# Kernel optimization log

Hardware: AMD Instinct MI355X
Metric: run time of the kernel (lower is better)

The kernel has to match this reference:

```python
import jax, jax.numpy as jnp
import numpy as np

B, HH, WW, C = 8, 56, 56, 192
DEPTH = 2
D_IN = 384      # ssm_ratio=2.0 * d_model
R = 12          # dt_rank = ceil(192/16)
HID = 768
L = HH * WW
EPS = 1e-5

PNAMES = ("norm1_w", "norm1_b", "in_proj_w", "conv_w", "conv_b", "x_proj_w",
          "dt_proj_w", "dt_proj_b", "A_log", "Ds", "out_norm_w", "out_norm_b",
          "out_proj_w", "norm2_w", "norm2_b", "fc1_w", "fc1_b", "fc2_w", "fc2_b")


def _mst_bfs_np(fm):
    """Per-image MST (Kruskal) on the 4-connected grid with cosine-distance
    edge weights mapped through exp (MinimumSpanningTree('Cosine', torch.exp)),
    then BFS from node 0. Returns (bfs order, parent-of-ordered-node)."""
    fm = np.asarray(fm, np.float32)
    Bn, H, W, Cc = fm.shape
    Ln = H * W
    idx_out = np.zeros((Bn, Ln), np.int32)
    par_out = np.zeros((Bn, Ln), np.int32)
    ids = np.arange(Ln).reshape(H, W)
    e_u = np.concatenate([ids[:, :-1].ravel(), ids[:-1, :].ravel()])
    e_v = np.concatenate([ids[:, 1:].ravel(), ids[1:, :].ravel()])
    for b in range(Bn):
        f = fm[b].reshape(Ln, Cc)
        nrm = np.linalg.norm(f, axis=1) + 1e-8
        cos = (f[e_u] * f[e_v]).sum(1) / (nrm[e_u] * nrm[e_v])
        wgt = np.exp(1.0 - cos)
        order = np.argsort(wgt, kind="stable")
        uf = np.arange(Ln)
        def find(a):
            while uf[a] != a:
                uf[a] = uf[uf[a]]
                a = uf[a]
            return a
        adj = [[] for _ in range(Ln)]
        cnt = 0
        for e in order:
            u, v = int(e_u[e]), int(e_v[e])
            ru, rv = find(u), find(v)
            if ru != rv:
                uf[ru] = rv
                adj[u].append(v)
                adj[v].append(u)
                cnt += 1
                if cnt == Ln - 1:
                    break
        bfs = np.zeros(Ln, np.int32)
        par = np.zeros(Ln, np.int32)
        visited = np.zeros(Ln, bool)
        visited[0] = True
        head, tail = 0, 1
        while head < tail:
            u = int(bfs[head])
            for v in adj[u]:
                if not visited[v]:
                    visited[v] = True
                    bfs[tail] = v
                    par[tail] = u
                    tail += 1
            head += 1
        idx_out[b] = bfs
        par_out[b] = par
    return idx_out, par_out


def _mst_bfs(x):
    shp = jax.ShapeDtypeStruct((x.shape[0], x.shape[1] * x.shape[2]), jnp.int32)
    return jax.pure_callback(_mst_bfs_np, (shp, shp), jax.lax.stop_gradient(x))


def _ln(x, w, b):
    mu = jnp.mean(x, -1, keepdims=True)
    var = jnp.mean((x - mu) ** 2, -1, keepdims=True)
    return (x - mu) * jax.lax.rsqrt(var + EPS) * w + b


def _tree_scan(feat, w, bfs_idx, bfs_par):
    # feat, w: (B, L, D); bfs_idx/bfs_par: (B, L) int32.
    # Pass 1 (leaf->root): S[p] += w[n] * S[n] in reverse BFS order.
    # Pass 2 (root->leaf): H[n] = S[n] + w[n] * (H[p] - w[n] * S[n]).
    Bn = feat.shape[0]
    bi = jnp.arange(Bn)

    def p1(S, np_):
        n, p = np_
        S = S.at[bi, p].add(w[bi, n] * S[bi, n])
        return S, None

    xs1 = (bfs_idx[:, 1:][:, ::-1].T, bfs_par[:, 1:][:, ::-1].T)
    S, _ = jax.lax.scan(p1, feat, xs1)

    def p2(Hc, np_):
        n, p = np_
        wn, sn = w[bi, n], S[bi, n]
        Hc = Hc.at[bi, n].set(sn + wn * (Hc[bi, p] - wn * sn))
        return Hc, None

    xs2 = (bfs_idx[:, 1:].T, bfs_par[:, 1:].T)
    Hh, _ = jax.lax.scan(p2, S, xs2)
    return Hh


def _layer(x, p, tree):
    bfs_idx, bfs_par = tree
    Bn = x.shape[0]
    # --- Tree_SSM branch (pre-norm) ---
    xn = _ln(x, p["norm1_w"], p["norm1_b"])
    xz = xn @ p["in_proj_w"].T                     # (B,H,W,2*D_IN)
    xs, z = jnp.split(xz, 2, axis=-1)
    xs = jax.lax.conv_general_dilated(
        xs, p["conv_w"], (1, 1), "SAME",
        dimension_numbers=("NHWC", "HWIO", "NHWC"),
        feature_group_count=D_IN) + p["conv_b"]    # depthwise 3x3
    u = jax.nn.silu(xs).reshape(Bn, L, D_IN)       # (B,L,D)
    x_dbl = u @ p["x_proj_w"].T                    # (B,L,R+2), d_state=1
    dts = jax.nn.softplus(x_dbl[..., :R] @ p["dt_proj_w"].T + p["dt_proj_b"])
    Bs, Cs = x_dbl[..., R:R + 1], x_dbl[..., R + 1:R + 2]
    A = -jnp.exp(p["A_log"][:, 0])                 # (D,)
    w = jnp.exp(dts * A)                           # edge decay to parent
    feat = dts * Bs * u                            # delta * B * u
    Hh = _tree_scan(feat, w, bfs_idx, bfs_par)
    y = (Cs * Hh + p["Ds"] * u).reshape(Bn, HH, WW, D_IN)
    y = _ln(y, p["out_norm_w"], p["out_norm_b"]) * jax.nn.silu(z)
    x = x + y @ p["out_proj_w"].T
    # --- MLP branch ---
    h = _ln(x, p["norm2_w"], p["norm2_b"])
    h = jax.nn.gelu(h @ p["fc1_w"].T + p["fc1_b"], approximate=False)
    return x + h @ p["fc2_w"].T + p["fc2_b"]


def setup_inputs() -> dict:
    key = jax.random.key(0)
    ks = jax.random.split(key, 12)
    n = jax.random.normal
    return {
        "x": n(ks[0], (B, HH, WW, C), jnp.float32),
        "norm1_w": jnp.ones((DEPTH, C)), "norm1_b": jnp.zeros((DEPTH, C)),
        "in_proj_w": n(ks[1], (DEPTH, 2 * D_IN, C)) * 0.02,
        "conv_w": n(ks[2], (DEPTH, 3, 3, 1, D_IN)) * 0.05,
        "conv_b": jnp.zeros((DEPTH, D_IN)),
        "x_proj_w": n(ks[3], (DEPTH, R + 2, D_IN)) * 0.02,
        "dt_proj_w": n(ks[4], (DEPTH, D_IN, R)) * 0.05,
        "dt_proj_b": n(ks[5], (DEPTH, D_IN)) * 0.1,
        "A_log": jnp.log(0.5 + jax.random.uniform(ks[6], (DEPTH, D_IN, 1))),
        "Ds": jax.random.uniform(ks[7], (DEPTH, D_IN)),
        "out_norm_w": jnp.ones((DEPTH, D_IN)), "out_norm_b": jnp.zeros((DEPTH, D_IN)),
        "out_proj_w": n(ks[8], (DEPTH, C, D_IN)) * 0.02,
        "norm2_w": jnp.ones((DEPTH, C)), "norm2_b": jnp.zeros((DEPTH, C)),
        "fc1_w": n(ks[9], (DEPTH, HID, C)) * 0.02, "fc1_b": jnp.zeros((DEPTH, HID)),
        "fc2_w": n(ks[10], (DEPTH, C, HID)) * 0.02, "fc2_b": jnp.zeros((DEPTH, C)),
        "fnorm_w": jnp.ones((C,)), "fnorm_b": jnp.zeros((C,)),
    }


def reference(x, norm1_w, norm1_b, in_proj_w, conv_w, conv_b, x_proj_w,
              dt_proj_w, dt_proj_b, A_log, Ds, out_norm_w, out_norm_b,
              out_proj_w, norm2_w, norm2_b, fc1_w, fc1_b, fc2_w, fc2_b,
              fnorm_w, fnorm_b):
    pvals = (norm1_w, norm1_b, in_proj_w, conv_w, conv_b, x_proj_w, dt_proj_w,
             dt_proj_b, A_log, Ds, out_norm_w, out_norm_b, out_proj_w, norm2_w,
             norm2_b, fc1_w, fc1_b, fc2_w, fc2_b)
    for i in range(DEPTH):
        pl = {k: v[i] for k, v in zip(PNAMES, pvals)}
        tree = _mst_bfs(x)  # input-adaptive MST, recomputed per layer
        x = _layer(x, pl, tree)
    return _ln(x, fnorm_w, fnorm_b)
```

## Files before the change

kernel.cpp:

```cpp
#include <hip/hip_runtime.h>
#include <math.h>

#define NB 8
#define NC 192
#define DIN 384
#define NL 3136
#define ROWS (NB*NL)
#define NE 6160
#define NHID 768

typedef unsigned short u16;
typedef unsigned int u32;
typedef unsigned long long u64;
typedef __attribute__((ext_vector_type(8))) short bh8;
typedef __attribute__((ext_vector_type(4))) float f4;

typedef __attribute__((address_space(1))) const void gl_as1;
typedef __attribute__((address_space(3))) void gl_as3;
#define GL16(g, l) __builtin_amdgcn_global_load_lds((gl_as1*)(const void*)(g), (gl_as3*)(void*)(l), 16, 0, 0)

__device__ __forceinline__ float wredsum(float v){
  v += __shfl_xor(v, 1, 64); v += __shfl_xor(v, 2, 64); v += __shfl_xor(v, 4, 64);
  v += __shfl_xor(v, 8, 64); v += __shfl_xor(v, 16, 64); v += __shfl_xor(v, 32, 64);
  return v;
}
__device__ __forceinline__ void edge_decode(int e, int& u, int& v){
  if (e < 3080){ int h = e/55, w = e - h*55; u = h*56 + w; v = u + 1; }
  else { int e2 = e - 3080; int h = e2/56, w = e2 - h*56; u = h*56 + w; v = u + 56; }
}
__device__ __forceinline__ float siluf(float x){ return x / (1.0f + expf(-x)); }
__device__ __forceinline__ float sofplus(float x){ return fmaxf(x, 0.0f) + log1pf(expf(-fabsf(x))); }
__device__ __forceinline__ float geluf(float x){ return 0.5f * x * (1.0f + erff(x * 0.70710678118654752f)); }
__device__ __forceinline__ u16 f2bf(float x){
  u32 u = __float_as_uint(x);
  u32 r = (u + 0x7fffu + ((u >> 16) & 1u)) >> 16;
  return (u16)r;
}
__device__ __forceinline__ float bf2f(u16 h){ return __uint_as_float(((u32)h) << 16); }

__global__ __launch_bounds__(256) void keysln_kernel(const float* __restrict__ x,
    const float* __restrict__ g, const float* __restrict__ bt,
    u16* __restrict__ lnout, u64* __restrict__ keys,
    const float* __restrict__ ipw, const float* __restrict__ opw,
    const float* __restrict__ f1w, const float* __restrict__ f2w,
    u16* __restrict__ ipo, u16* __restrict__ opo, u16* __restrict__ f1o, u16* __restrict__ f2o){
  int bid = blockIdx.x;
  int lane = threadIdx.x & 63;
  if (bid < 6272){
    int gw = (int)((bid * 256u + threadIdx.x) >> 6);
    const float* r = x + (size_t)gw * NC;
    float v[3]; float s = 0.f;
#pragma unroll
    for (int j = 0; j < 3; ++j){ v[j] = r[lane + 64*j]; s += v[j]; }
    s = wredsum(s);
    float mu = s * (1.0f / NC);
    float q = 0.f;
#pragma unroll
    for (int j = 0; j < 3; ++j){ float dd = v[j] - mu; q += dd*dd; }
    q = wredsum(q);
    float rs = rsqrtf(q * (1.0f / NC) + 1e-5f);
    u16* o = lnout + (size_t)gw * NC;
#pragma unroll
    for (int j = 0; j < 3; ++j){
      int dch = lane + 64*j;
      o[dch] = f2bf((v[j] - mu) * rs * g[dch] + bt[dch]);
    }
  } else if (bid < 18592){
    int gw = (int)(((bid - 6272) * 256u + threadIdx.x) >> 6);
    if (gw >= NB * NE) return;
    int b = gw / NE, e = gw - b * NE;
    int u, v; edge_decode(e, u, v);
    const float* ru = x + ((size_t)b * NL + u) * NC;
    const float* rv = x + ((size_t)b * NL + v) * NC;
    float s = 0.f, su = 0.f, sv = 0.f;
#pragma unroll
    for (int j = 0; j < 3; ++j){
      float a = ru[lane + 64*j], c = rv[lane + 64*j];
      s += a * c; su += a * a; sv += c * c;
    }
    s = wredsum(s);
    su = wredsum(su);
    sv = wredsum(sv);
    if (lane == 0){
      float nu = sqrtf(su) + 1e-8f;
      float nv = sqrtf(sv) + 1e-8f;
      float cosv = s / (nu * nv);
      float wgt = expf(1.0f - cosv);
      keys[(size_t)b*NE + e] = ((u64)__float_as_uint(wgt) << 32) | (u64)(u32)e;
    }
  } else {
    int wb = bid - 18592;
    const float* W; u16* o; int K; int nk; int base;
    if (wb < 576){ W = ipw; o = ipo; K = 192; nk = 768*192; base = wb; }
    else if (wb < 864){ W = opw; o = opo; K = 384; nk = 192*384; base = wb - 576; }
    else if (wb < 1440){ W = f1w; o = f1o; K = 192; nk = 768*192; base = wb - 864; }
    else { W = f2w; o = f2o; K = 768; nk = 192*768; base = wb - 1440; }
    int i = base*256 + threadIdx.x;
    if (i >= nk) return;
    int r = i / K, c = i - r*K;
    float v = W[i];
    u16 hi = f2bf(v);
    o[(size_t)r * 2 * K + c] = hi;
    o[(size_t)r * 2 * K + K + c] = f2bf(v - bf2f(hi));
  }
}

__device__ void tree_body(char* sm, int b, const u64* __restrict__ keys_g,
      int* __restrict__ order_g, int* __restrict__ parpos_g, int* __restrict__ pos_g,
      int* __restrict__ lvl_g, int* __restrict__ nlev_g){
  const int t = threadIdx.x;
  const int NT = 256;
  u64* best   = (u64*)sm;
  u16* parent = (u16*)(sm + 25088);
  u16* comp   = (u16*)(sm + 31360);
  u16* mstU   = (u16*)(sm + 37632);
  u16* mstV   = (u16*)(sm + 43904);
  u32* cnts   = (u32*)(sm + 56448);
  u16* adjl4  = (u16*)sm;
  u32* deg    = (u32*)(sm + 25088);
  u32* fr     = (u32*)(sm + 37632);
  u16* ppos   = (u16*)(sm + 50176);

  const u64* kb = keys_g + (size_t)b * NE;
  for (int v = t; v < NL; v += NT) parent[v] = (u16)v;
  if (t == 0){ cnts[0] = 0; cnts[3] = 0xffffffffu; }
  __syncthreads();

  u32 gpass = 0;
  for (int round = 0; round < 24; ++round){
    for (int it = 0; it < 12; ++it){
      bool ch = false;
      for (int c0 = 0; c0 < NL; c0 += NT*4){
        int vv[4]; u16 pv[4]; int nb2 = 0;
#pragma unroll
        for (int j = 0; j < 4; ++j){ int v = c0 + t + j*NT; if (v < NL){ vv[nb2] = v; pv[nb2] = parent[v]; ++nb2; } }
        u16 gp[4];
        for (int j = 0; j < nb2; ++j) gp[j] = parent[pv[j]];
        for (int j = 0; j < nb2; ++j){ if (gp[j] != pv[j]){ parent[vv[j]] = gp[j]; ch = true; } }
      }
      bool docheck = (it & 1);
      if (docheck && ch) cnts[3] = gpass;
      __syncthreads();
      if (docheck){
        u32 seen = cnts[3];
        __syncthreads();
        u32 cur = gpass; ++gpass;
        if (seen != cur) break;
      }
    }
    for (int v = t; v < NL; v += NT){ comp[v] = parent[v]; best[v] = ~0ull; }
    if (t == 0) cnts[2] = 0;
    __syncthreads();
    for (int c0 = 0; c0 < NE; c0 += NT*8){
      int ee[8]; int eu[8], ev[8]; u16 cu[8], cv[8]; u64 kk[8]; int nb2 = 0;
#pragma unroll
      for (int j = 0; j < 8; ++j){
        int e = c0 + t + j*NT;
        if (e < NE){ ee[nb2] = e; int u, v; edge_decode(e, u, v); eu[nb2] = u; ev[nb2] = v; ++nb2; }
      }
      for (int j = 0; j < nb2; ++j){ cu[j] = comp[eu[j]]; cv[j] = comp[ev[j]]; }
      for (int j = 0; j < nb2; ++j){ kk[j] = kb[ee[j]]; }
      for (int j = 0; j < nb2; ++j){
        if (cu[j] != cv[j]){
          atomicMin(&best[cu[j]], kk[j]);
          atomicMin(&best[cv[j]], kk[j]);
        }
      }
    }
    __syncthreads();
    for (int c0 = 0; c0 < NL; c0 += NT*4){
      int rr[4]; u64 bk[4]; int nb2 = 0;
#pragma unroll
      for (int j = 0; j < 4; ++j){ int r = c0 + t + j*NT; if (r < NL){ rr[nb2] = r; ++nb2; } }
      u16 cr[4];
      for (int j = 0; j < nb2; ++j) cr[j] = comp[rr[j]];
      for (int j = 0; j < nb2; ++j) bk[j] = (cr[j] == (u16)rr[j]) ? best[rr[j]] : ~0ull;
      int uu[4], vv2[4]; u16 ru2[4], rv2[4];
      for (int j = 0; j < nb2; ++j){
        if (bk[j] != ~0ull){ int e = (int)(u32)bk[j]; edge_decode(e, uu[j], vv2[j]); }
      }
      for (int j = 0; j < nb2; ++j){
        if (bk[j] != ~0ull){ ru2[j] = comp[uu[j]]; rv2[j] = comp[vv2[j]]; }
      }
      for (int j = 0; j < nb2; ++j){
        if (bk[j] != ~0ull){
          int r = rr[j];
          u16 other = (ru2[j] == (u16)r) ? rv2[j] : ru2[j];
          bool mutual = (best[other] == bk[j]);
          if (!mutual || (u16)r < other){
            parent[r] = other;
            u32 id = atomicAdd(&cnts[0], 1);
            mstU[id] = (u16)uu[j]; mstV[id] = (u16)vv2[j];
            cnts[2] = 1;
          }
        }
      }
    }
    __syncthreads();
    if (cnts[0] >= (u32)(NL - 1) || cnts[2] == 0) break;
  }
  __syncthreads();

  const int nm = NL - 1;
  for (int v = t; v < NL; v += NT){
    deg[v] = 0;
    *(u64*)&adjl4[v*4] = 0xffffffffffffffffull;
  }
  __syncthreads();
  for (int c0 = 0; c0 < nm; c0 += NT*4){
    int uu[4], vv2[4]; int nb2 = 0;
#pragma unroll
    for (int j = 0; j < 4; ++j){
      int i = c0 + t + j*NT;
      if (i < nm){ uu[nb2] = mstU[i]; vv2[nb2] = mstV[i]; ++nb2; }
    }
    for (int j = 0; j < nb2; ++j){
      u32 s1 = atomicAdd(&deg[uu[j]], 1); adjl4[uu[j]*4 + s1] = (u16)vv2[j];
      u32 s2 = atomicAdd(&deg[vv2[j]], 1); adjl4[vv2[j]*4 + s2] = (u16)uu[j];
    }
  }
  __syncthreads();

  if (t == 0){
    fr[0] = 0u | (0xffffu << 16);
    ppos[0] = 0;
    cnts[1] = 1;
    lvl_g[b*3200 + 0] = 0; lvl_g[b*3200 + 1] = 1;
  }
  __syncthreads();
  if (t < 64){
    int flo = 0, fhi = 1, d = 1;
    while (fhi < NL){
      for (int base2 = flo; base2 < fhi; base2 += 64){
        int idx = base2 + t;
        if (idx < fhi){
          u32 f = fr[idx];
          int u = (int)(f & 0xffffu), pn = (int)(f >> 16);
          u64 four = *(const u64*)&adjl4[u*4];
#pragma unroll
          for (int j = 0; j < 4; ++j){
            int v = (int)((four >> (16*j)) & 0xffffu);
            if (v != 0xffff && v != pn){
              u32 pos = atomicAdd(&cnts[1], 1);
              fr[pos] = (u32)v | ((u32)u << 16);
              ppos[pos] = (u16)idx;
            }
          }
        }
        asm volatile("s_waitcnt lgkmcnt(0)" ::: "memory");
      }
      int nf = (int)cnts[1];
      if (t == 0) lvl_g[b*3200 + d + 1] = nf;
      flo = fhi; fhi = nf; ++d;
      if (nf == flo) break;
    }
    if (t == 0) nlev_g[b] = d;
  }
  __syncthreads();

  for (int p = t; p < NL; p += NT){
    u32 f = fr[p];
    int node = (int)(f & 0xffffu);
    order_g[b*NL + p] = node;
    parpos_g[b*NL + p] = (int)ppos[p];
    pos_g[b*NL + node] = p;
  }
}

__device__ void inproj_body(char* sm, int bid, const u16* __restrict__ Ap, const u16* __restrict__ Wp,
                            float* __restrict__ Cm, float* __restrict__ C2){
  const int K = 192, K2 = 384;
  short* Ah = (short*)sm;
  short* Wh = (short*)(sm + 16384);
  short* Wl = (short*)(sm + 32768);
  const int bn = (bid % 6) * 128, bm = (bid / 6) * 128;
  const int tid = threadIdx.x, lane = tid & 63, wid = tid >> 6;
  const int wr = wid >> 1, wc = wid & 1;
  f4 acc[4][4];
#pragma unroll
  for (int mf = 0; mf < 4; ++mf)
#pragma unroll
    for (int nf = 0; nf < 4; ++nf) acc[mf][nf] = (f4){0.f,0.f,0.f,0.f};

  for (int k0 = 0; k0 < K; k0 += 64){
#pragma unroll
    for (int j = 0; j < 4; ++j){
      int isb = wid*4 + j;
      int r = isb*8 + (lane >> 3);
      int c = lane & 7;
      const u16* src = Ap + (size_t)(bm + r) * K + k0 + ((c ^ (r & 7)) << 3);
      GL16(src, &Ah[isb*512]);
    }
#pragma unroll
    for (int j = 0; j < 4; ++j){
      int isb = wid*4 + j;
      int r = isb*8 + (lane >> 3);
      int c = lane & 7;
      const u16* src = Wp + (size_t)(bn + r) * K2 + k0 + ((c ^ (r & 7)) << 3);
      GL16(src,     &Wh[isb*512]);
      GL16(src + K, &Wl[isb*512]);
    }
    __syncthreads();
#pragma unroll
    for (int kk = 0; kk < 2; ++kk){
      bh8 whf[4], wlf[4], ahf[4];
#pragma unroll
      for (int nf = 0; nf < 4; ++nf){
        int rw = wc*64 + nf*16 + (lane & 15);
        int c = kk*4 + (lane >> 4);
        int ad = rw*64 + ((c ^ (rw & 7)) * 8);
        whf[nf] = *(const bh8*)&Wh[ad];
        wlf[nf] = *(const bh8*)&Wl[ad];
      }
#pragma unroll
      for (int mf = 0; mf < 4; ++mf){
        int ra = wr*64 + mf*16 + (lane & 15);
        int c = kk*4 + (lane >> 4);
        int ad = ra*64 + ((c ^ (ra & 7)) * 8);
        ahf[mf] = *(const bh8*)&Ah[ad];
      }
#pragma unroll
      for (int mf = 0; mf < 4; ++mf)
#pragma unroll
        for (int nf = 0; nf < 4; ++nf){
          acc[mf][nf] = __builtin_amdgcn_mfma_f32_16x16x32_bf16(ahf[mf], whf[nf], acc[mf][nf], 0, 0, 0);
          acc[mf][nf] = __builtin_amdgcn_mfma_f32_16x16x32_bf16(ahf[mf], wlf[nf], acc[mf][nf], 0, 0, 0);
        }
    }
    __syncthreads();
  }
  const int cb = bn + wc*64;
#pragma unroll
  for (int mf = 0; mf < 4; ++mf){
    int row = bm + wr*64 + mf*16 + (lane >> 4)*4;
#pragma unroll
    for (int nf = 0; nf < 4; ++nf){
      int col = cb + nf*16 + (lane & 15);
#pragma unroll
      for (int r = 0; r < 4; ++r){
        float v = acc[mf][nf][r];
        float* op = (col < 384) ? Cm : C2;
        int oc = (col < 384) ? col : col - 384;
        op[(size_t)(row + r) * 384 + oc] = v;
      }
    }
  }
}

__global__ __launch_bounds__(256) void fused_tree_inproj(
    const u64* __restrict__ keysg, int* __restrict__ ordg, int* __restrict__ ppg,
    int* __restrict__ posg, int* __restrict__ lvlg, int* __restrict__ nlvg,
    const u16* __restrict__ Ap, const u16* __restrict__ Wp,
    float* __restrict__ Cm, float* __restrict__ C2){
  __shared__ __align__(16) char sm[62736];
  int bid = blockIdx.x;
  if (bid < 8){
    tree_body(sm, bid, keysg, ordg, ppg, posg, lvlg, nlvg);
  } else {
    inproj_body(sm, bid - 8, Ap, Wp, Cm, C2);
  }
}

__global__ __launch_bounds__(256) void sched_conv_kernel(
    const int* __restrict__ lvl_g, const int* __restrict__ nlev_g,
    u32* __restrict__ wsched_g, int* __restrict__ nwin_g,
    const float* __restrict__ xs, const float* __restrict__ cw,
    const float* __restrict__ cb, float* __restrict__ u){
  __shared__ int lvls[3200];
  int bid = blockIdx.x;
  if (bid < 8){
    int b = bid;
    int tid = threadIdx.x;
    int d = nlev_g[b];
    for (int i = tid; i <= d; i += 256) lvls[i] = lvl_g[b*3200 + i];
    __syncthreads();
    if (tid >= 64) return;
    int lane = tid;
    u32* su = wsched_g + (size_t)b*6528;
    u32* sd = su + 3264;
    int nk = d - 1;
    for (int pass = 0; pass < 2; ++pass){
      u32* out = pass ? sd : su;
      int carry = 0;
      for (int c0 = 0; c0 < nk; c0 += 64){
        int kk = c0 + lane;
        bool valid = kk < nk;
        int lo = 0, hi = 0, wc = 0;
        if (valid){
          int dd = pass ? (1 + kk) : (d - 1 - kk);
          lo = lvls[dd]; hi = lvls[dd+1];
          wc = (hi - lo + 63) >> 6;
        }
        int inc = wc;
        for (int off = 1; off < 64; off <<= 1){
          int v = __shfl_up(inc, off, 64);
          if (lane >= off) inc += v;
        }
        int excl = carry + inc - wc;
        if (valid){
          for (int w = 0; w < wc; ++w){
            int base2 = lo + (w << 6);
            u32 e = (u32)base2 | ((u32)hi << 16);
            if (base2 + 64 >= hi) e |= 0x80000000u;
            out[excl + w] = e;
          }
        }
        carry += __shfl(inc, 63, 64);
      }
      if (lane == 0) nwin_g[b*2 + pass] = carry;
    }
  } else {
    int idx = (bid - 8) * 256 + threadIdx.x;
    if (idx >= ROWS * 96) return;
    int q = idx % 96; int l = idx / 96;
    int b = l / NL; int hw = l - b * NL; int h = hw / 56; int wcc = hw - h * 56;
    int c4 = q * 4;
    float4 acc = *(const float4*)(cb + c4);
#pragma unroll
    for (int kh = 0; kh < 3; ++kh){
      int hh = h + kh - 1; if (hh < 0 || hh >= 56) continue;
#pragma unroll
      for (int kw = 0; kw < 3; ++kw){
        int wwc = wcc + kw - 1; if (wwc < 0 || wwc >= 56) continue;
        float4 iv = *(const float4*)(xs + ((size_t)(b * NL + hh*56 + wwc)) * DIN + c4);
        float4 wv = *(const float4*)(cw + (size_t)(kh*3 + kw) * DIN + c4);
        acc.x += iv.x * wv.x; acc.y += iv.y * wv.y; acc.z += iv.z * wv.z; acc.w += iv.w * wv.w;
      }
    }
    float4 o; o.x = siluf(acc.x); o.y = siluf(acc.y); o.z = siluf(acc.z); o.w = siluf(acc.w);
    *(float4*)(u + (size_t)l * DIN + c4) = o;
  }
}

template<int D, bool BF16OUT>
__global__ __launch_bounds__(256) void ln_kernel(const float* __restrict__ in, const float* __restrict__ g,
                                                 const float* __restrict__ bt, void* __restrict__ outv){
  int gw = (int)((blockIdx.x * 256u + threadIdx.x) >> 6);
  int lane = threadIdx.x & 63;
  if (gw >= ROWS) return;
  constexpr int J = D / 64;
  const float* r = in + (size_t)gw * D;
  float v[J]; float s = 0.f;
#pragma unroll
  for (int j = 0; j < J; ++j){ v[j] = r[lane + 64*j]; s += v[j]; }
  s = wredsum(s);
  float mu = s * (1.0f / D);
  float q = 0.f;
#pragma unroll
  for (int j = 0; j < J; ++j){ float dd = v[j] - mu; q += dd*dd; }
  q = wredsum(q);
  float rs = rsqrtf(q * (1.0f / D) + 1e-5f);
  if (BF16OUT){
    u16* o = (u16*)outv + (size_t)gw * D;
#pragma unroll
    for (int j = 0; j < J; ++j){
      int dch = lane + 64*j;
      float y = (v[j] - mu) * rs * g[dch] + bt[dch];
      o[dch] = f2bf(y);
    }
  } else {
    float* o = (float*)outv + (size_t)gw * D;
#pragma unroll
    for (int j = 0; j < J; ++j){ int dch = lane + 64*j; o[dch] = (v[j] - mu) * rs * g[dch] + bt[dch]; }
  }
}

template<int BN, bool BIAS, int ACT, bool RESID, bool OBF16, bool DUALOUT>
__global__ __launch_bounds__(256) void mgemm_kernel(
    const u16* __restrict__ Ap, const u16* __restrict__ Wp,
    const float* __restrict__ bias, const float* __restrict__ resid,
    float* __restrict__ Cm, float* __restrict__ C2, int M, int N, int K){
  static_assert(BN == 64 || BN == 128, "BN");
  constexpr int WT = (BN == 128) ? 64 : 32;
  constexpr int NF = WT / 16;
  __shared__ short Ah[128*64];
  __shared__ short Wh[BN*64], Wl[BN*64];
  const int bm = blockIdx.y * 128, bn = blockIdx.x * BN;
  const int tid = threadIdx.x, lane = tid & 63, wid = tid >> 6;
  const int wr = wid >> 1, wc = wid & 1;
  const int K2 = 2 * K;
  f4 acc[4][NF];
#pragma unroll
  for (int mf = 0; mf < 4; ++mf)
#pragma unroll
    for (int nf = 0; nf < NF; ++nf) acc[mf][nf] = (f4){0.f,0.f,0.f,0.f};

  for (int k0 = 0; k0 < K; k0 += 64){
#pragma unroll
    for (int j = 0; j < 4; ++j){
      int isb = wid*4 + j;
      int r = isb*8 + (lane >> 3);
      int c = lane & 7;
      const u16* src = Ap + (size_t)(bm + r) * K + k0 + ((c ^ (r & 7)) << 3);
      GL16(src, &Ah[isb*512]);
    }
#pragma unroll
    for (int j = 0; j < BN/32; ++j){
      int isb = wid*(BN/32) + j;
      int r = isb*8 + (lane >> 3);
      int c = lane & 7;
      const u16* src = Wp + (size_t)(bn + r) * K2 + k0 + ((c ^ (r & 7)) << 3);
      GL16(src,     &Wh[isb*512]);
      GL16(src + K, &Wl[isb*512]);
    }
    __syncthreads();
#pragma unroll
    for (int kk = 0; kk < 2; ++kk){
      bh8 whf[NF], wlf[NF], ahf[4];
#pragma unroll
      for (int nf = 0; nf < NF; ++nf){
        int rw = wc*WT + nf*16 + (lane & 15);
        int c = kk*4 + (lane >> 4);
        int ad = rw*64 + ((c ^ (rw & 7)) * 8);
        whf[nf] = *(const bh8*)&Wh[ad];
        wlf[nf] = *(const bh8*)&Wl[ad];
      }
#pragma unroll
      for (int mf = 0; mf < 4; ++mf){
        int ra = wr*64 + mf*16 + (lane & 15);
        int c = kk*4 + (lane >> 4);
        int ad = ra*64 + ((c ^ (ra & 7)) * 8);
        ahf[mf] = *(const bh8*)&Ah[ad];
      }
#pragma unroll
      for (int mf = 0; mf < 4; ++mf)
#pragma unroll
        for (int nf = 0; nf < NF; ++nf){
          acc[mf][nf] = __builtin_amdgcn_mfma_f32_16x16x32_bf16(ahf[mf], whf[nf], acc[mf][nf], 0, 0, 0);
          acc[mf][nf] = __builtin_amdgcn_mfma_f32_16x16x32_bf16(ahf[mf], wlf[nf], acc[mf][nf], 0, 0, 0);
        }
    }
    __syncthreads();
  }
  const int cb = bn + wc*WT;
#pragma unroll
  for (int mf = 0; mf < 4; ++mf){
    int row = bm + wr*64 + mf*16 + (lane >> 4)*4;
#pragma unroll
    for (int nf = 0; nf < NF; ++nf){
      int col = cb + nf*16 + (lane & 15);
#pragma unroll
      for (int r = 0; r < 4; ++r){
        float v = acc[mf][nf][r];
        if (BIAS) v += bias[col];
        if (ACT == 1) v = geluf(v);
        if (RESID) v += resid[(size_t)(row + r) * N + col];
        if (DUALOUT){
          float* op = (col < 384) ? Cm : C2;
          int oc = (col < 384) ? col : col - 384;
          op[(size_t)(row + r) * 384 + oc] = v;
        } else if (OBF16){
          u16* op = (u16*)Cm;
          op[(size_t)(row + r) * N + col] = f2bf(v);
        } else {
          Cm[(size_t)(row + r) * N + col] = v;
        }
      }
    }
  }
}

__global__ __launch_bounds__(256) void xdbl_kernel(const float* __restrict__ u,
    const float* __restrict__ xpw, const float* __restrict__ dtw_g,
    const float* __restrict__ dtb, const float* __restrict__ alog, const int* __restrict__ pos_g,
    float* __restrict__ wout, float* __restrict__ fout, float* __restrict__ csout){
  __shared__ float xw[14*384];
  __shared__ float dw[384*12];
  __shared__ float db[384];
  __shared__ float An[384];
  int t = threadIdx.x;
  for (int i = t; i < 14*384; i += 256) xw[i] = xpw[i];
  for (int i = t; i < 384*12; i += 256) dw[i] = dtw_g[i];
  for (int i = t; i < 384; i += 256){ db[i] = dtb[i]; An[i] = -expf(alog[i]); }
  __syncthreads();
  int wave = t >> 6, lane = t & 63;
  int row0 = blockIdx.x * 16 + wave * 4;
  for (int rr = 0; rr < 4; ++rr){
    int m = row0 + rr;
    int b = m / NL;
    int pos = pos_g[m];
    size_t orow = ((size_t)b * NL + pos) * DIN;
    const float* ur = u + (size_t)m * DIN;
    float u6[6];
#pragma unroll
    for (int j = 0; j < 6; ++j) u6[j] = ur[lane + 64*j];
    float xd[14];
#pragma unroll
    for (int r = 0; r < 14; ++r){
      float p = 0.f;
#pragma unroll
      for (int j = 0; j < 6; ++j) p += u6[j] * xw[r*384 + lane + 64*j];
      xd[r] = wredsum(p);
    }
    float Bs = xd[12], Cv = xd[13];
#pragma unroll
    for (int j = 0; j < 6; ++j){
      int dch = lane + 64*j;
      float pre = db[dch];
#pragma unroll
      for (int r = 0; r < 12; ++r) pre += xd[r] * dw[dch*12 + r];
      float dts = sofplus(pre);
      float wv = expf(dts * An[dch]);
      float fv = dts * Bs * u6[j];
      wout[orow + dch] = wv;
      fout[orow + dch] = fv;
    }
    if (lane == 0) csout[m] = Cv;
  }
}

__global__ __launch_bounds__(256) void wtr_kernel(const float* __restrict__ in, float* __restrict__ out){
  __shared__ float tile[64][65];
  int blk = blockIdx.x;
  int b = blk / (49*6);
  int r = blk - b*(49*6);
  int pt = r / 6, ct = r - pt*6;
  int t = threadIdx.x;
  int tr = t >> 6, lane = t & 63;
  const float* src = in + ((size_t)b*NL + (size_t)pt*64) * DIN + ct*64;
#pragma unroll
  for (int k = 0; k < 16; ++k){
    int rr = tr + k*4;
    tile[rr][lane] = src[(size_t)rr*DIN + lane];
  }
  __syncthreads();
  float* dst = out + ((size_t)b*DIN + (size_t)ct*64) * NL + (size_t)pt*64;
#pragma unroll
  for (int k = 0; k < 16; ++k){
    int cc = tr + k*4;
    dst[(size_t)cc*NL + lane] = tile[lane][cc];
  }
}

template<bool UP>
__device__ __forceinline__ void sweep_run(const u32* __restrict__ sc, int nw,
    float* __restrict__ Sp, const float* __restrict__ wbase, const int* __restrict__ pg, int lane){
  if (nw <= 0) return;
  u32 d0 = sc[lane];
  u32 d1 = sc[64 + lane];
  int curch = 0;
  float wA = 0.f, wB = 0.f; int pA = 0, pB = 0;
  int baseA = 0, hiA = 0, baseB = 0, hiB = 0;
  u32 eA = 0, eB = 0; bool aA = false, aB = false;
  {
    u32 dc = __shfl(d0, 0, 64);
    baseA = (int)(dc & 0xffffu); hiA = (int)((dc >> 16) & 0x7fffu); eA = dc >> 31;
    int p = baseA + lane; aA = p < hiA;
    if (aA){ wA = wbase[p]; pA = pg[p]; }
  }
  if (nw > 1){
    u32 dc = __shfl(d0, 1, 64);
    baseB = (int)(dc & 0xffffu); hiB = (int)((dc >> 16) & 0x7fffu); eB = dc >> 31;
    int p = baseB + lane; aB = p < hiB;
    if (aB){ wB = wbase[p]; pB = pg[p]; }
  }
  for (int iw = 0; iw < nw; ++iw){
    int ch = iw >> 6;
    if (ch != curch){ d0 = d1; d1 = sc[(ch + 1)*64 + lane]; curch = ch; }
    float wN = 0.f; int pN = 0; int baseN = 0, hiN = 0; u32 eN = 0; bool aN = false;
    int iw2 = iw + 2;
    if (iw2 < nw){
      int ch2 = iw2 >> 6;
      u32 dc2 = __shfl((ch2 == curch) ? d0 : d1, iw2 & 63, 64);
      baseN = (int)(dc2 & 0xffffu); hiN = (int)((dc2 >> 16) & 0x7fffu); eN = dc2 >> 31;
      int p = baseN + lane; aN = p < hiN;
      if (aN){ wN = wbase[p]; pN = pg[p]; }
    }
    int p = baseA + lane;
    if (aA){
      if (UP){
        float s = Sp[p];
        atomicAdd(&Sp[pA], wA * s);
      } else {
        float s = Sp[p]; float h = Sp[pA];
        Sp[p] = s + wA * (h - wA * s);
      }
    }
    if (eA){
      asm volatile("s_waitcnt lgkmcnt(0)" ::: "memory");
    }
    baseA = baseB; hiA = hiB; aA = aB; wA = wB; pA = pB; eA = eB;
    baseB = baseN; hiB = hiN; aB = aN; wB = wN; pB = pN; eB = eN;
  }
}

__global__ __launch_bounds__(256) void sweep8_kernel(const float* __restrict__ featp, const float* __restrict__ wtr,
    float* __restrict__ Hp, const int* __restrict__ parpos_g,
    const u32* __restrict__ wsched_g, const int* __restrict__ nwin_g){
  __shared__ float S[4*NL];
  int blk = blockIdx.x;
  int b = blk & 7, q = blk >> 3;
  int t = threadIdx.x, lane = t & 63, wv = t >> 6;
  const int* pg = parpos_g + b*NL;
  const float* fbase = featp + (size_t)b*NL*DIN + q*4;
  const float* wbase = wtr + ((size_t)b*DIN + q*4 + wv) * NL;
  float*       hbase = Hp    + (size_t)b*NL*DIN + q*4;
  for (int i = t; i < NL; i += 256){
    float4 f = *(const float4*)(fbase + (size_t)i*DIN);
    S[0*NL + i] = f.x; S[1*NL + i] = f.y; S[2*NL + i] = f.z; S[3*NL + i] = f.w;
  }
  __syncthreads();
  float* Sp = &S[wv*NL];

  const u32* su = wsched_g + (size_t)b*6528;
  const u32* sd = su + 3264;
  int nwu = nwin_g[b*2], nwd = nwin_g[b*2 + 1];
  sweep_run<true>(su, nwu, Sp, wbase, pg, lane);
  sweep_run<false>(sd, nwd, Sp, wbase, pg, lane);

  __syncthreads();
  for (int i = t; i < NL; i += 256){
    float4 o;
    o.x = S[0*NL + i]; o.y = S[1*NL + i]; o.z = S[2*NL + i]; o.w = S[3*NL + i];
    *(float4*)(hbase + (size_t)i*DIN) = o;
  }
}

__global__ __launch_bounds__(256) void ynorm_kernel(const float* __restrict__ Hp, const float* __restrict__ u,
    const float* __restrict__ z, const float* __restrict__ Cs, const int* __restrict__ order_g,
    const float* __restrict__ Ds, const float* __restrict__ g, const float* __restrict__ bt,
    u16* __restrict__ out){
  int gw = (int)((blockIdx.x * 256u + threadIdx.x) >> 6);
  int lane = threadIdx.x & 63;
  if (gw >= ROWS) return;
  int b = gw / NL;
  int node = order_g[gw];
  size_t nrow = (size_t)b * NL + node;
  float Cv = Cs[nrow];
  const float* hr = Hp + (size_t)gw * DIN;
  const float* ur = u + nrow * DIN;
  const float* zr = z + nrow * DIN;
  float y[6]; float s = 0.f;
#pragma unroll
  for (int j = 0; j < 6; ++j){
    int dch = lane + 64*j;
    y[j] = Cv * hr[dch] + Ds[dch] * ur[dch];
    s += y[j];
  }
  s = wredsum(s);
  float mu = s * (1.0f / DIN);
  float q = 0.f;
#pragma unroll
  for (int j = 0; j < 6; ++j){ float dd = y[j] - mu; q += dd*dd; }
  q = wredsum(q);
  float rs = rsqrtf(q * (1.0f / DIN) + 1e-5f);
  u16* o = out + nrow * DIN;
#pragma unroll
  for (int j = 0; j < 6; ++j){
    int dch = lane + 64*j;
    float yn = (y[j] - mu) * rs * g[dch] + bt[dch];
    float v = yn * siluf(zr[dch]);
    o[dch] = f2bf(v);
  }
}

extern "C" void kernel_launch(void* const* d_in, const int* in_sizes, int n_in,
                              void* d_out, int out_size, void* d_ws, size_t ws_size,
                              hipStream_t stream){
  const float* x_in       = (const float*)d_in[0];
  const float* norm1_w    = (const float*)d_in[1];
  const float* norm1_b    = (const float*)d_in[2];
  const float* in_proj_w  = (const float*)d_in[3];
  const float* conv_w     = (const float*)d_in[4];
  const float* conv_b     = (const float*)d_in[5];
  const float* x_proj_w   = (const float*)d_in[6];
  const float* dt_proj_w  = (const float*)d_in[7];
  const float* dt_proj_b  = (const float*)d_in[8];
  const float* A_log      = (const float*)d_in[9];
  const float* Ds         = (const float*)d_in[10];
  const float* out_norm_w = (const float*)d_in[11];
  const float* out_norm_b = (const float*)d_in[12];
  const float* out_proj_w = (const float*)d_in[13];
  const float* norm2_w    = (const float*)d_in[14];
  const float* norm2_b    = (const float*)d_in[15];
  const float* fc1_w      = (const float*)d_in[16];
  const float* fc1_b      = (const float*)d_in[17];
  const float* fc2_w      = (const float*)d_in[18];
  const float* fc2_b      = (const float*)d_in[19];
  const float* fnorm_w    = (const float*)d_in[20];
  const float* fnorm_b    = (const float*)d_in[21];

  float* ws = (float*)d_ws;
  float* X     = ws + 0;
  u16*   bufAh = (u16*)(ws + 4816896);
  float* bufZ  = ws + 9633792;
  float* bufW  = ws + 19267584;
  float* bufU  = ws + 28901376;
  float* bufF  = ws + 38535168;
  u16*   Gp    = (u16*)bufU;
  float* Csb   = ws + 48168960;
  int*   ordg  = (int*)(ws + 48194048);
  int*   ppg   = (int*)(ws + 48219136);
  int*   lvlg  = (int*)(ws + 48244224);
  int*   nlvg  = (int*)(ws + 48269824);
  u64*   keysg = (u64*)(ws + 48269832);
  u16*   ipWp  = (u16*)(ws + 48393480);
  u16*   opWp  = (u16*)(ws + 48540936);
  u16*   fc1Wp = (u16*)(ws + 48614664);
  u16*   fc2Wp = (u16*)(ws + 48762120);
  int*   posg  = (int*)(ws + 48909576);
  float* wtrp  = ws + 48934664;
  u32*   wschg = (u32*)(ws + 58568456);
  int*   nwing = (int*)(ws + 58620680);

  hipMemcpyAsync(X, x_in, (size_t)ROWS * NC * sizeof(float), hipMemcpyDeviceToDevice, stream);

  for (int i = 0; i < 2; ++i){
    keysln_kernel<<<20608, 256, 0, stream>>>(X, norm1_w + i*NC, norm1_b + i*NC, bufAh, keysg,
                                             in_proj_w + (size_t)i*NHID*NC, out_proj_w + (size_t)i*NC*DIN,
                                             fc1_w + (size_t)i*NHID*NC, fc2_w + (size_t)i*NC*NHID,
                                             ipWp, opWp, fc1Wp, fc2Wp);

    fused_tree_inproj<<<8 + 6*196, 256, 0, stream>>>(keysg, ordg, ppg, posg, lvlg, nlvg,
                                                     bufAh, ipWp, bufF, bufZ);

    sched_conv_kernel<<<8 + (ROWS*96)/256, 256, 0, stream>>>(lvlg, nlvg, wschg, nwing,
                                                             bufF, conv_w + (size_t)i*9*DIN, conv_b + i*DIN, bufU);

    xdbl_kernel<<<ROWS/16, 256, 0, stream>>>(bufU, x_proj_w + (size_t)i*14*DIN, dt_proj_w + (size_t)i*DIN*12,
                                             dt_proj_b + i*DIN, A_log + i*DIN, posg, bufW, bufF, Csb);

    wtr_kernel<<<8*49*6, 256, 0, stream>>>(bufW, wtrp);

    sweep8_kernel<<<NB*96, 256, 0, stream>>>(bufF, wtrp, bufF, ppg, wschg, nwing);

    ynorm_kernel<<<ROWS/4, 256, 0, stream>>>(bufF, bufU, bufZ, Csb, ordg, Ds + i*DIN,
                                             out_norm_w + i*DIN, out_norm_b + i*DIN, (u16*)bufW);

    mgemm_kernel<64,false,0,true,false,false><<<dim3(3,196), 256, 0, stream>>>((u16*)bufW, opWp, nullptr, X, X, nullptr, ROWS, 192, 384);

    ln_kernel<192,true><<<ROWS/4, 256, 0, stream>>>(X, norm2_w + i*NC, norm2_b + i*NC, bufAh);
    mgemm_kernel<128,true,1,false,true,false><<<dim3(6,196), 256, 0, stream>>>(bufAh, fc1Wp, fc1_b + i*NHID, nullptr, (float*)Gp, nullptr, ROWS, NHID, 192);
    mgemm_kernel<64,true,0,true,false,false><<<dim3(3,196), 256, 0, stream>>>(Gp, fc2Wp, fc2_b + i*NC, X, X, nullptr, ROWS, 192, 768);
  }

  ln_kernel<192,false><<<ROWS/4, 256, 0, stream>>>(X, fnorm_w, fnorm_b, d_out);
}
```

Baseline: 1.413 ms.

## Replace single-wave BFS with parallel Euler-tour depth computation for tree ordering

```diff
diff --git a/kernel.cpp b/kernel.cpp
--- a/kernel.cpp
+++ b/kernel.cpp
@@ -118,8 +118,6 @@
   u32* cnts   = (u32*)(sm + 56448);
   u16* adjl4  = (u16*)sm;
   u32* deg    = (u32*)(sm + 25088);
-  u32* fr     = (u32*)(sm + 37632);
-  u16* ppos   = (u16*)(sm + 50176);
 
   const u64* kb = keys_g + (size_t)b * NE;
   for (int v = t; v < NL; v += NT) parent[v] = (u16)v;
@@ -221,49 +219,232 @@
   }
   __syncthreads();
 
-  if (t == 0){
-    fr[0] = 0u | (0xffffu << 16);
-    ppos[0] = 0;
-    cnts[1] = 1;
-    lvl_g[b*3200 + 0] = 0; lvl_g[b*3200 + 1] = 1;
-  }
-  __syncthreads();
-  if (t < 64){
-    int flo = 0, fhi = 1, d = 1;
-    while (fhi < NL){
-      for (int base2 = flo; base2 < fhi; base2 += 64){
-        int idx = base2 + t;
-        if (idx < fhi){
-          u32 f = fr[idx];
-          int u = (int)(f & 0xffffu), pn = (int)(f >> 16);
-          u64 four = *(const u64*)&adjl4[u*4];
-#pragma unroll
-          for (int j = 0; j < 4; ++j){
-            int v = (int)((four >> (16*j)) & 0xffffu);
-            if (v != 0xffff && v != pn){
-              u32 pos = atomicAdd(&cnts[1], 1);
-              fr[pos] = (u32)v | ((u32)u << 16);
-              ppos[pos] = (u16)idx;
-            }
-          }
-        }
-        asm volatile("s_waitcnt lgkmcnt(0)" ::: "memory");
-      }
-      int nf = (int)cnts[1];
-      if (t == 0) lvl_g[b*3200 + d + 1] = nf;
-      flo = fhi; fhi = nf; ++d;
-      if (nf == flo) break;
-    }
-    if (t == 0) nlev_g[b] = d;
-  }
-  __syncthreads();
-
-  for (int p = t; p < NL; p += NT){
-    u32 f = fr[p];
-    int node = (int)(f & 0xffffu);
-    order_g[b*NL + p] = node;
-    parpos_g[b*NL + p] = (int)ppos[p];
-    pos_g[b*NL + node] = p;
+  const int NARC = 2 * (NL - 1);
+  u16*  arcB  = (u16*)(sm + 37632);
+  u16*  nxt   = (u16*)(sm + 43908);
+  u16*  rankA = (u16*)(sm + 25088);
+  short* S16  = (short*)(sm + 43908);
+  u16*  parA  = (u16*)(sm + 43908);
+  u32*  hist  = (u32*)(sm + 25088);
+  u16*  posA  = (u16*)(sm + 37632);
+  u16*  dep   = (u16*)(sm + 56448);
+  u32*  wsum  = (u32*)(sm + 62720);
+  const int lane = t & 63, wv = t >> 6;
+
+  {
+    int dloc[13]; int st = 0;
+#pragma unroll
+    for (int j = 0; j < 13; ++j){
+      int v = t*13 + j;
+      dloc[j] = (v < NL) ? (int)deg[v] : 0;
+      st += dloc[j];
+    }
+    int inc = st;
+#pragma unroll
+    for (int off = 1; off < 64; off <<= 1){
+      int sh = __shfl_up(inc, off, 64);
+      if (lane >= off) inc += sh;
+    }
+    if (lane == 63) wsum[wv] = (u32)inc;
+    __syncthreads();
+    int woff = 0;
+    for (int k = 0; k < 4; ++k) if (k < wv) woff += (int)wsum[k];
+    int run = woff + inc - st;
+#pragma unroll
+    for (int j = 0; j < 13; ++j){
+      int v = t*13 + j;
+      if (v < NL) arcB[v] = (u16)run;
+      run += dloc[j];
+    }
+    if (t == 255) arcB[NL] = (u16)run;
+  }
+  __syncthreads();
+
+  for (int idx = t; idx < NL*4; idx += NT){
+    int u = idx >> 2, sl = idx & 3;
+    int v = (int)adjl4[idx];
+    if (v != 0xffff){
+      int dv = (int)(arcB[v+1] - arcB[v]);
+      int rs = 0;
+#pragma unroll
+      for (int j = 0; j < 4; ++j) if ((int)adjl4[v*4+j] == u) rs = j;
+      int ns = rs + 1; if (ns >= dv) ns = 0;
+      nxt[arcB[u] + sl] = (u16)(arcB[v] + ns);
+    }
+  }
+  __syncthreads();
+  for (int a = t; a < NARC; a += NT){
+    if (nxt[a] == 0) nxt[a] = 0xffff;
+  }
+  __syncthreads();
+
+  for (int a = t; a < NARC; a += NT) rankA[a] = (nxt[a] == 0xffff) ? (u16)0 : (u16)1;
+  __syncthreads();
+  for (int it = 0; it < 13; ++it){
+    u16 nn[25], rr2[25];
+#pragma unroll
+    for (int k = 0; k < 25; ++k){
+      int a = t + k*NT;
+      nn[k] = 0xfffe; rr2[k] = 0;
+      if (a < NARC){
+        u16 n = nxt[a];
+        if (n != 0xffff){ rr2[k] = rankA[n]; nn[k] = nxt[n]; }
+      }
+    }
+    __syncthreads();
+#pragma unroll
+    for (int k = 0; k < 25; ++k){
+      int a = t + k*NT;
+      if (a < NARC && nn[k] != 0xfffe){
+        rankA[a] = (u16)(rankA[a] + rr2[k]);
+        nxt[a] = nn[k];
+      }
+    }
+    __syncthreads();
+  }
+
+  for (int idx = t; idx < NL*4; idx += NT){
+    int u = idx >> 2, sl = idx & 3;
+    int v = (int)adjl4[idx];
+    if (v != 0xffff){
+      int a  = arcB[u] + sl;
+      int rs = 0;
+#pragma unroll
+      for (int j = 0; j < 4; ++j) if ((int)adjl4[v*4+j] == u) rs = j;
+      int ar = arcB[v] + rs;
+      bool down = rankA[a] > rankA[ar];
+      int pt = (NARC - 1) - (int)rankA[a];
+      S16[pt] = down ? (short)1 : (short)-1;
+    }
+  }
+  __syncthreads();
+
+  {
+    int base = t * 25;
+    int vals[25]; int st = 0;
+#pragma unroll
+    for (int j = 0; j < 25; ++j){
+      int i = base + j;
+      vals[j] = (i < NARC) ? (int)S16[i] : 0;
+      st += vals[j];
+    }
+    int inc = st;
+#pragma unroll
+    for (int off = 1; off < 64; off <<= 1){
+      int sh = __shfl_up(inc, off, 64);
+      if (lane >= off) inc += sh;
+    }
+    if (lane == 63) wsum[wv] = (u32)inc;
+    __syncthreads();
+    int woff = 0;
+    for (int k = 0; k < 4; ++k) if (k < wv) woff += (int)wsum[k];
+    int run = woff + inc - st;
+#pragma unroll
+    for (int j = 0; j < 25; ++j){
+      int i = base + j;
+      run += vals[j];
+      if (i < NARC) S16[i] = (short)run;
+    }
+  }
+  __syncthreads();
+
+  if (t == 0) dep[0] = 0;
+  for (int idx = t; idx < NL*4; idx += NT){
+    int u = idx >> 2, sl = idx & 3;
+    int v = (int)adjl4[idx];
+    if (v != 0xffff){
+      int a  = arcB[u] + sl;
+      int rs = 0;
+#pragma unroll
+      for (int j = 0; j < 4; ++j) if ((int)adjl4[v*4+j] == u) rs = j;
+      int ar = arcB[v] + rs;
+      if (rankA[a] > rankA[ar]){
+        int pt = (NARC - 1) - (int)rankA[a];
+        dep[v] = (u16)S16[pt];
+      }
+    }
+  }
+  __syncthreads();
+
+  if (t == 0) parA[0] = 0;
+  for (int idx = t; idx < NL*4; idx += NT){
+    int u = idx >> 2, sl = idx & 3;
+    int v = (int)adjl4[idx];
+    if (v != 0xffff){
+      int a  = arcB[u] + sl;
+      int rs = 0;
+#pragma unroll
+      for (int j = 0; j < 4; ++j) if ((int)adjl4[v*4+j] == u) rs = j;
+      int ar = arcB[v] + rs;
+      if (rankA[a] > rankA[ar]) parA[v] = (u16)u;
+    }
+  }
+  __syncthreads();
+
+  for (int i = t; i < NL; i += NT) hist[i] = 0;
+  __syncthreads();
+  int mloc = 0;
+  for (int v = t; v < NL; v += NT){
+    int dv = (int)dep[v];
+    atomicAdd(&hist[dv], 1u);
+    if (dv > mloc) mloc = dv;
+  }
+#pragma unroll
+  for (int off = 1; off < 64; off <<= 1){
+    int o = __shfl_xor(mloc, off, 64);
+    if (o > mloc) mloc = o;
+  }
+  __syncthreads();
+  if (lane == 0) wsum[wv] = (u32)mloc;
+  __syncthreads();
+  int maxd = 0;
+  for (int k = 0; k < 4; ++k){ int x = (int)wsum[k]; if (x > maxd) maxd = x; }
+  int nlev = maxd + 1;
+  __syncthreads();
+
+  {
+    int hloc[13]; int st = 0;
+#pragma unroll
+    for (int j = 0; j < 13; ++j){
+      int i2 = t*13 + j;
+      hloc[j] = (i2 < NL) ? (int)hist[i2] : 0;
+      st += hloc[j];
+    }
+    int inc = st;
+#pragma unroll
+    for (int off = 1; off < 64; off <<= 1){
+      int sh = __shfl_up(inc, off, 64);
+      if (lane >= off) inc += sh;
+    }
+    if (lane == 63) wsum[wv] = (u32)inc;
+    __syncthreads();
+    int woff = 0;
+    for (int k = 0; k < 4; ++k) if (k < wv) woff += (int)wsum[k];
+    int run = woff + inc - st;
+#pragma unroll
+    for (int j = 0; j < 13; ++j){
+      int i2 = t*13 + j;
+      int h = hloc[j];
+      if (i2 < NL) hist[i2] = (u32)run;
+      run += h;
+    }
+  }
+  __syncthreads();
+  for (int i = t; i < nlev; i += NT) lvl_g[b*3200 + i] = (int)hist[i];
+  if (t == 0){ lvl_g[b*3200 + nlev] = NL; nlev_g[b] = nlev; }
+  __syncthreads();
+
+  for (int v = t; v < NL; v += NT){
+    u32 p = atomicAdd(&hist[(int)dep[v]], 1u);
+    posA[v] = (u16)p;
+  }
+  __syncthreads();
+
+  for (int v = t; v < NL; v += NT){
+    int p = (int)posA[v];
+    order_g[b*NL + p] = v;
+    pos_g[b*NL + v] = p;
+    parpos_g[b*NL + p] = (int)posA[parA[v]];
   }
 }
 
```

New measurement: 1.293 ms, median of 2. 8.5% less time.
